# Kernel optimization log

Measured on AMD Instinct MI355X. Metric: run time of the kernel, lower is better.

Reference implementation:

```python
import jax, jax.numpy as jnp
import numpy as np
import math

B, T, C, H = 4, 2048, 1024, 16
D = C // H  # head dim = 64


def setup_inputs() -> dict:
    key = jax.random.key(0)
    ks = jax.random.split(key, 5)
    scale = 0.02
    x = jax.random.normal(ks[0], (B, T, C), dtype=jnp.float32)
    # torch nn.Linear(n_embd, 3*n_embd): weight [3C, C]; we store transposed [C, 3C]
    W_kqv = jax.random.normal(ks[1], (C, 3 * C), dtype=jnp.float32) * scale
    b_kqv = jnp.zeros((3 * C,), dtype=jnp.float32)
    W_proj = jax.random.normal(ks[2], (C, C), dtype=jnp.float32) * scale
    b_proj = jnp.zeros((C,), dtype=jnp.float32)
    padding_mask = jnp.ones((B, T), dtype=jnp.int32)  # 1 = valid token
    return {"x": x, "W_kqv": W_kqv, "b_kqv": b_kqv, "W_proj": W_proj,
            "b_proj": b_proj, "padding_mask": padding_mask}


def reference(x, W_kqv, b_kqv, W_proj, b_proj, padding_mask):
    Bx, Tx, Cx = x.shape
    kqv = x @ W_kqv + b_kqv                      # [B,T,3C]
    # original splits as k, q, v (in that order)
    k, q, v = jnp.split(kqv, 3, axis=2)
    def heads(t):
        return t.reshape(Bx, Tx, H, D).transpose(0, 2, 1, 3)  # [B,H,T,D]
    k, q, v = heads(k), heads(q), heads(v)
    att = jnp.einsum('bhqd,bhkd->bhqk', q, k) * (1.0 / math.sqrt(D))  # [B,H,T,T]
    causal = jnp.tril(jnp.ones((Tx, Tx), dtype=bool))[None, None]     # [1,1,T,T]
    valid = causal & (padding_mask[:, None, None, :] != 0)            # [B,1,T,T] broadcast
    neg_inf = jnp.finfo(att.dtype).min
    att = jnp.where(valid, att, neg_inf)
    att = jax.nn.softmax(att, axis=-1)
    y = jnp.einsum('bhqk,bhkd->bhqd', att, v)    # [B,H,T,D]
    y = y.transpose(0, 2, 1, 3).reshape(Bx, Tx, Cx)
    return y @ W_proj + b_proj
```

## Files before the change

### kernel.cpp

```cpp
#include <hip/hip_runtime.h>


typedef short bf16x8 __attribute__((ext_vector_type(8)));
typedef float floatx4 __attribute__((ext_vector_type(4)));

#define MFMA16(a, b, c) __builtin_amdgcn_mfma_f32_16x16x32_bf16(a, b, c, 0, 0, 0)

#define ASYNC_COPY16(gp, lp)                                                   \
  __builtin_amdgcn_global_load_lds(                                            \
      (__attribute__((address_space(1))) void*)(gp),                           \
      (__attribute__((address_space(3))) void*)(lp), 16, 0, 0)

#define DRAIN_VMCNT() asm volatile("s_waitcnt vmcnt(0)" ::: "memory")
#define WAIT_VMCNT6() asm volatile("s_waitcnt vmcnt(6)" ::: "memory")

#if defined(__has_builtin)
#if __has_builtin(__builtin_amdgcn_exp2f)
#define EXP2(x) __builtin_amdgcn_exp2f(x)
#endif
#endif
#ifndef EXP2
#define EXP2(x) exp2f(x)
#endif

__device__ __forceinline__ short f2bf(float f) {
  union { float f; unsigned u; } c;
  c.f = f;
  unsigned r = c.u + 0x7fffu + ((c.u >> 16) & 1u);
  return (short)(r >> 16);
}

__global__ __launch_bounds__(256) void prep(const float* __restrict__ x,
                                            short* __restrict__ xb,
                                            const float* __restrict__ Wkqv,
                                            short* __restrict__ Wkqvt,
                                            const float* __restrict__ Wproj,
                                            short* __restrict__ Wprojt) {
  __shared__ float buf[64][65];
  const int t = threadIdx.x;
  const int bx = blockIdx.x;
  if (bx < 8192) {
    int i = (bx * 256 + t) * 4;
    float4 v = *(const float4*)&x[i];
    short4 o;
    o.x = f2bf(v.x); o.y = f2bf(v.y); o.z = f2bf(v.z); o.w = f2bf(v.w);
    *(short4*)&xb[i] = o;
    return;
  }
  const int tb = bx - 8192;
  const int nb = tb & 63, kb = tb >> 6;
  const float* in;
  short* out;
  int N, n0;
  if (nb < 48) { in = Wkqv; out = Wkqvt; N = 3072; n0 = nb * 64; }
  else         { in = Wproj; out = Wprojt; N = 1024; n0 = (nb - 48) * 64; }
  const int k0 = kb * 64;
#pragma unroll
  for (int i = 0; i < 4; ++i) {
    int s = t + i * 256;
    int row = s >> 4, c4 = (s & 15) * 4;
    float4 v = *(const float4*)&in[(size_t)(k0 + row) * N + n0 + c4];
    buf[row][c4] = v.x; buf[row][c4 + 1] = v.y;
    buf[row][c4 + 2] = v.z; buf[row][c4 + 3] = v.w;
  }
  __syncthreads();
#pragma unroll
  for (int i = 0; i < 2; ++i) {
    int u = t + i * 256;
    int rn = u >> 3, ch = (u & 7) * 8;
    short tmp[8];
#pragma unroll
    for (int j = 0; j < 8; ++j) tmp[j] = f2bf(buf[ch + j][rn]);
    *(uint4*)&out[(size_t)(n0 + rn) * 1024 + k0 + ch] = *(uint4*)tmp;
  }
}

template <int MODE>
__global__ __launch_bounds__(512, 2) void gemm_ph256(const short* __restrict__ A,
                                                     const short* __restrict__ Bt,
                                                     const float* __restrict__ bias,
                                                     void* __restrict__ Cout,
                                                     int M, int N, int K) {
  __shared__ short smem[73728];
  const int tid = threadIdx.x;
  const int lane = tid & 63;
  const int wv = tid >> 6;
  const int l15 = lane & 15, quad = lane >> 4;
  const int xr = l15 & 7;
  const int m0 = blockIdx.y * 128, n0 = blockIdx.x * 256;
  const int wm = (wv >> 2) * 64, wn = (wv & 3) * 64;
  const int NT = K >> 6;

  floatx4 acc[4][4] = {};

#define STAGE_A(kt, bs, j)                                                     \
  { int c_ = (j) * 512 + tid;                                                  \
    int r_ = c_ >> 3, ch_ = (c_ & 7) ^ (r_ & 7);                               \
    ASYNC_COPY16(&A[(size_t)(m0 + r_) * K + (kt) * 64 + ch_ * 8],              \
                 &smem[(bs) * 8192 + c_ * 8]); }
#define STAGE_B(kt, bs, j)                                                     \
  { int c_ = (j) * 512 + tid;                                                  \
    int r_ = c_ >> 3, ch_ = (c_ & 7) ^ (r_ & 7);                               \
    ASYNC_COPY16(&Bt[(size_t)(n0 + r_) * K + (kt) * 64 + ch_ * 8],             \
                 &smem[24576 + (bs) * 16384 + c_ * 8]); }

  STAGE_A(0, 0, 0); STAGE_A(0, 0, 1);
  STAGE_B(0, 0, 0); STAGE_B(0, 0, 1); STAGE_B(0, 0, 2); STAGE_B(0, 0, 3);
  STAGE_A(1, 1, 0); STAGE_A(1, 1, 1);
  STAGE_B(1, 1, 0); STAGE_B(1, 1, 1); STAGE_B(1, 1, 2); STAGE_B(1, 1, 3);
  WAIT_VMCNT6();
  __builtin_amdgcn_s_barrier();

  int cur = 0, nxt = 2;
  for (int kt = 0; kt < NT; ++kt) {
    const bool st = (kt + 2 < NT);
    const short* Asr = &smem[cur * 8192];
    const short* Bsr = &smem[24576 + cur * 16384];

    if (st) { STAGE_A(kt + 2, nxt, 0); STAGE_A(kt + 2, nxt, 1); STAGE_B(kt + 2, nxt, 0); }
    bf16x8 af[4][2], bf0[2][2];
#pragma unroll
    for (int mi = 0; mi < 4; ++mi)
#pragma unroll
      for (int s = 0; s < 2; ++s)
        af[mi][s] = *(const bf16x8*)
            &Asr[(wm + mi * 16 + l15) * 64 + (((s * 4 + quad) ^ xr) * 8)];
#pragma unroll
    for (int nj = 0; nj < 2; ++nj)
#pragma unroll
      for (int s = 0; s < 2; ++s)
        bf0[nj][s] = *(const bf16x8*)
            &Bsr[(wn + nj * 16 + l15) * 64 + (((s * 4 + quad) ^ xr) * 8)];
    __builtin_amdgcn_s_setprio(1);
#pragma unroll
    for (int s = 0; s < 2; ++s)
#pragma unroll
      for (int mi = 0; mi < 4; ++mi)
#pragma unroll
        for (int nj = 0; nj < 2; ++nj)
          acc[mi][nj] = MFMA16(af[mi][s], bf0[nj][s], acc[mi][nj]);
    __builtin_amdgcn_s_setprio(0);
    __builtin_amdgcn_s_barrier();

    if (st) { STAGE_B(kt + 2, nxt, 1); STAGE_B(kt + 2, nxt, 2); STAGE_B(kt + 2, nxt, 3); }
    bf16x8 bf1[2][2];
#pragma unroll
    for (int nj = 0; nj < 2; ++nj)
#pragma unroll
      for (int s = 0; s < 2; ++s)
        bf1[nj][s] = *(const bf16x8*)
            &Bsr[(wn + (2 + nj) * 16 + l15) * 64 + (((s * 4 + quad) ^ xr) * 8)];
    __builtin_amdgcn_s_setprio(1);
#pragma unroll
    for (int s = 0; s < 2; ++s)
#pragma unroll
      for (int mi = 0; mi < 4; ++mi)
#pragma unroll
        for (int nj = 0; nj < 2; ++nj)
          acc[mi][2 + nj] = MFMA16(af[mi][s], bf1[nj][s], acc[mi][2 + nj]);
    __builtin_amdgcn_s_setprio(0);
    if (st) { WAIT_VMCNT6(); } else { DRAIN_VMCNT(); }
    __builtin_amdgcn_s_barrier();
    cur = (cur == 2) ? 0 : cur + 1;
    nxt = (nxt == 2) ? 0 : nxt + 1;
  }
#undef STAGE_A
#undef STAGE_B

  if (MODE == 0) {
    float* outf = (float*)Cout;
#pragma unroll
    for (int ni = 0; ni < 4; ++ni) {
      int col = n0 + wn + ni * 16 + l15;
      float bv = bias[col];
#pragma unroll
      for (int mi = 0; mi < 4; ++mi) {
#pragma unroll
        for (int rr = 0; rr < 4; ++rr) {
          int row = m0 + wm + mi * 16 + quad * 4 + rr;
          outf[(size_t)row * N + col] = acc[mi][ni][rr] + bv;
        }
      }
    }
  } else {
    short* outs = (short*)Cout;
    const size_t QOFF = (size_t)64 * 2048 * 64;
    const int sec = n0 >> 10;
    short* Es = smem;
    if (sec < 2) {
#pragma unroll
      for (int ni = 0; ni < 4; ++ni) {
        int c = wn + ni * 16 + l15;
        float bv = bias[n0 + c];
#pragma unroll
        for (int mi = 0; mi < 4; ++mi) {
          int r0 = wm + mi * 16 + quad * 4;
#pragma unroll
          for (int rr = 0; rr < 4; ++rr) {
            int r = r0 + rr;
            Es[r * 256 + (c ^ (((r >> 2) & 3) << 4))] = f2bf(acc[mi][ni][rr] + bv);
          }
        }
      }
    } else {
#pragma unroll
      for (int ni = 0; ni < 4; ++ni) {
        int c = wn + ni * 16 + l15;
        float bv = bias[n0 + c];
#pragma unroll
        for (int mi = 0; mi < 4; ++mi) {
          int r0 = wm + mi * 16 + quad * 4;
#pragma unroll
          for (int rr = 0; rr < 4; ++rr) {
            int r = r0 + rr;
            Es[c * 128 + (r ^ ((c & 7) << 3))] = f2bf(acc[mi][ni][rr] + bv);
          }
        }
      }
    }
    __syncthreads();
    if (sec < 2) {
#pragma unroll
      for (int jj = 0; jj < 8; ++jj) {
        int idx = jj * 512 + tid;
        int rr2 = idx >> 5;
        int cc2 = (idx & 31) * 8;
        uint4 v = *(const uint4*)&Es[rr2 * 256 + (cc2 ^ (((rr2 >> 2) & 3) << 4))];
        int colg = n0 + cc2;
        int hh = (colg >> 6) & 15, dd = colg & 63;
        int row = m0 + rr2, bb = row >> 11, tt = row & 2047;
        *(uint4*)(outs + (size_t)sec * QOFF +
                  (((size_t)(bb * 16 + hh) * 2048 + tt) * 64 + dd)) = v;
      }
    } else {
#pragma unroll
      for (int jj = 0; jj < 8; ++jj) {
        int idx = jj * 512 + tid;
        int cd = idx >> 4;
        int rb = (idx & 15) * 8;
        uint4 v = *(const uint4*)&Es[cd * 128 + (rb ^ ((cd & 7) << 3))];
        int colg = n0 + cd;
        int hh = (colg >> 6) & 15, dd = colg & 63;
        int trow = m0 + rb, bb = trow >> 11, tt = trow & 2047;
        *(uint4*)(outs + 2 * QOFF +
                  ((size_t)(bb * 16 + hh) * 64 + dd) * 2048 + tt) = v;
      }
    }
  }
}

__global__ __launch_bounds__(256, 3) void attn_flash8(const short* __restrict__ Qd,
                                                      const short* __restrict__ Kd,
                                                      const short* __restrict__ Vd,
                                                      const int* __restrict__ pmask,
                                                      short* __restrict__ y) {
  constexpr int T = 2048, C = 1024;
  __shared__ short Ks[2][64 * 64];
  __shared__ short Vs[2][64 * 64];
  __shared__ short Ps[4][32][64];

  const int tid = threadIdx.x;
  const int lane = tid & 63, w = tid >> 6;
  const int l15 = lane & 15, quad = lane >> 4;
  const int xr = l15 & 7;
  const int lin = blockIdx.x;
  const int qb = 15 - (lin >> 6);
  const int bh = lin & 63;
  const int b = bh >> 4, h = bh & 15;
  const short* Qb = Qd + (size_t)bh * T * 64;
  const short* Kb = Kd + (size_t)bh * T * 64;
  const short* Vb = Vd + (size_t)bh * 64 * T;
  const int* pmi = &pmask[b * T];
  const int q0 = qb * 128;
  const int nt = (q0 >> 6) + 2;

  const float SCALE2 = 0.18033688011112042f;

#define STAGE_KV(t, buf)                                                       \
  {                                                                            \
    const short* ksrc_ = Kb + (size_t)((t) * 64) * 64;                         \
    const short* vsrc_ = Vb + (t) * 64;                                        \
    _Pragma("unroll")                                                          \
    for (int j_ = 0; j_ < 2; ++j_) {                                           \
      int c_ = j_ * 256 + tid;                                                 \
      int r_ = c_ >> 3, cc_ = (c_ & 7) ^ (r_ & 7);                             \
      ASYNC_COPY16(ksrc_ + r_ * 64 + cc_ * 8, &Ks[buf][c_ * 8]);               \
      ASYNC_COPY16(vsrc_ + (size_t)r_ * T + cc_ * 8, &Vs[buf][c_ * 8]);        \
    }                                                                          \
  }

  bf16x8 qf[2][2];
#pragma unroll
  for (int mi = 0; mi < 2; ++mi) {
    const short* qp = Qb + (size_t)(q0 + w * 32 + mi * 16 + l15) * 64;
    qf[mi][0] = *(const bf16x8*)&qp[quad * 8];
    qf[mi][1] = *(const bf16x8*)&qp[32 + quad * 8];
  }

  floatx4 Oacc[2][4] = {};
  float lpart[2] = {};

  STAGE_KV(0, 0);
  DRAIN_VMCNT();
  __syncthreads();

  int cur = 0;
#pragma unroll 1
  for (int t = 0; t < nt; ++t) {
    const int k0 = t * 64;
    if (t + 1 < nt) STAGE_KV(t + 1, cur ^ 1);

    floatx4 Sacc[2][4] = {};
#pragma unroll
    for (int s = 0; s < 2; ++s) {
#pragma unroll
      for (int n4 = 0; n4 < 4; ++n4) {
        bf16x8 bK = *(const bf16x8*)
            &Ks[cur][(n4 * 16 + l15) * 64 + (((s * 4 + quad) ^ xr) * 8)];
        Sacc[0][n4] = MFMA16(bK, qf[0][s], Sacc[0][n4]);
        Sacc[1][n4] = MFMA16(bK, qf[1][s], Sacc[1][n4]);
      }
    }

    if (k0 < q0) {
#pragma unroll
      for (int n4 = 0; n4 < 4; ++n4) {
        int4 pm4 = *(const int4*)&pmi[k0 + n4 * 16 + quad * 4];
        float pb[4];
        pb[0] = pm4.x ? 0.0f : -3.0e38f;
        pb[1] = pm4.y ? 0.0f : -3.0e38f;
        pb[2] = pm4.z ? 0.0f : -3.0e38f;
        pb[3] = pm4.w ? 0.0f : -3.0e38f;
#pragma unroll
        for (int mi = 0; mi < 2; ++mi) {
          float p[4];
#pragma unroll
          for (int rr = 0; rr < 4; ++rr) {
            p[rr] = EXP2(fmaf(Sacc[mi][n4][rr], SCALE2, pb[rr]));
            lpart[mi] += p[rr];
          }
          unsigned lo, hi;
          asm("v_cvt_pk_bf16_f32 %0, %1, %2" : "=v"(lo) : "v"(p[0]), "v"(p[1]));
          asm("v_cvt_pk_bf16_f32 %0, %1, %2" : "=v"(hi) : "v"(p[2]), "v"(p[3]));
          uint2 pk; pk.x = lo; pk.y = hi;
          *(uint2*)&Ps[w][mi * 16 + l15]
                      [((n4 * 2 + (quad >> 1)) ^ xr) * 8 + (quad & 1) * 4] = pk;
        }
      }
    } else {
#pragma unroll
      for (int n4 = 0; n4 < 4; ++n4) {
        int4 pm4 = *(const int4*)&pmi[k0 + n4 * 16 + quad * 4];
        float pb[4];
        pb[0] = pm4.x ? 0.0f : -3.0e38f;
        pb[1] = pm4.y ? 0.0f : -3.0e38f;
        pb[2] = pm4.z ? 0.0f : -3.0e38f;
        pb[3] = pm4.w ? 0.0f : -3.0e38f;
        const int colb = n4 * 16 + quad * 4;
#pragma unroll
        for (int mi = 0; mi < 2; ++mi) {
          const int rowb = (q0 - k0) + w * 32 + mi * 16 + l15;
          float p[4];
#pragma unroll
          for (int rr = 0; rr < 4; ++rr) {
            float v = EXP2(fmaf(Sacc[mi][n4][rr], SCALE2, pb[rr]));
            if (colb + rr > rowb) v = 0.f;
            p[rr] = v;
            lpart[mi] += v;
          }
          unsigned lo, hi;
          asm("v_cvt_pk_bf16_f32 %0, %1, %2" : "=v"(lo) : "v"(p[0]), "v"(p[1]));
          asm("v_cvt_pk_bf16_f32 %0, %1, %2" : "=v"(hi) : "v"(p[2]), "v"(p[3]));
          uint2 pk; pk.x = lo; pk.y = hi;
          *(uint2*)&Ps[w][mi * 16 + l15]
                      [((n4 * 2 + (quad >> 1)) ^ xr) * 8 + (quad & 1) * 4] = pk;
        }
      }
    }

#pragma unroll
    for (int ks2 = 0; ks2 < 2; ++ks2) {
      const int pco = (((ks2 * 4 + quad) ^ xr) * 8);
      bf16x8 ap0 = *(const bf16x8*)&Ps[w][l15][pco];
      bf16x8 ap1 = *(const bf16x8*)&Ps[w][16 + l15][pco];
#pragma unroll
      for (int nd = 0; nd < 4; ++nd) {
        bf16x8 bV = *(const bf16x8*)
            &Vs[cur][(nd * 16 + l15) * 64 + (((ks2 * 4 + quad) ^ xr) * 8)];
        Oacc[0][nd] = MFMA16(ap0, bV, Oacc[0][nd]);
        Oacc[1][nd] = MFMA16(ap1, bV, Oacc[1][nd]);
      }
    }

    DRAIN_VMCNT();
    __syncthreads();
    cur ^= 1;
  }
#undef STAGE_KV

#pragma unroll
  for (int mi = 0; mi < 2; ++mi) {
    float s = lpart[mi];
    s += __shfl_xor(s, 16, 64);
    s += __shfl_xor(s, 32, 64);
    float inv_l[4];
#pragma unroll
    for (int rr = 0; rr < 4; ++rr)
      inv_l[rr] = 1.0f / __shfl(s, quad * 4 + rr, 16);
#pragma unroll
    for (int n = 0; n < 4; ++n) {
      int dcol = n * 16 + l15;
#pragma unroll
      for (int rr = 0; rr < 4; ++rr) {
        int rowq = q0 + w * 32 + mi * 16 + quad * 4 + rr;
        y[((size_t)(b * T + rowq)) * C + h * 64 + dcol] =
            f2bf(Oacc[mi][n][rr] * inv_l[rr]);
      }
    }
  }
}

extern "C" void kernel_launch(void* const* d_in, const int* in_sizes, int n_in,
                              void* d_out, int out_size, void* d_ws, size_t ws_size,
                              hipStream_t stream) {
  constexpr int B = 4, T = 2048, C = 1024;
  constexpr int M = B * T;
  constexpr int N1 = 3 * C;

  const float* x      = (const float*)d_in[0];
  const float* W_kqv  = (const float*)d_in[1];
  const float* b_kqv  = (const float*)d_in[2];
  const float* W_proj = (const float*)d_in[3];
  const float* b_proj = (const float*)d_in[4];
  const int*   pmask  = (const int*)d_in[5];
  float* out = (float*)d_out;

  const size_t QOFF = (size_t)64 * T * 64;

  short* xb     = (short*)d_ws;
  short* Wkqvt  = xb + (size_t)M * C;
  short* Wprojt = Wkqvt + (size_t)N1 * C;
  short* qkv    = Wprojt + (size_t)C * C;
  short* yb     = xb;

  short* Kd = qkv;
  short* Qd = qkv + QOFF;
  short* Vd = qkv + 2 * QOFF;

  prep<<<dim3(8192 + 1024), 256, 0, stream>>>(x, xb, W_kqv, Wkqvt, W_proj, Wprojt);

  gemm_ph256<2><<<dim3(N1 / 256, M / 128), 512, 0, stream>>>(xb, Wkqvt, b_kqv, Kd, M, N1, C);

  attn_flash8<<<dim3(1024), 256, 0, stream>>>(Qd, Kd, Vd, pmask, yb);

  gemm_ph256<0><<<dim3(C / 256, M / 128), 512, 0, stream>>>(yb, Wprojt, b_proj, out, M, C, C);
}
```

Before: 252.3 us.

## Keep softmax probabilities in registers via permlane swaps and add 128-tile output GEMM

The attention kernel no longer writes probabilities to a per-wave LDS buffer and reads them back for the PV MFMA. It reshuffles them in registers with v_permlane32_swap and shuffles, computes O transposed, and stores packed bf16 rows. A runtime probe (sem1) picks the swap semantics. The output projection now uses a new 128x128 double-buffered GEMM with 256 threads in place of the 256-wide, 512-thread triple-buffered one. This trades LDS traffic for cross-lane ops and changes the projection's tiling and occupancy.

Result: slower. 258.6 us (+2.5%).

```diff
diff --git a/kernel.cpp b/kernel.cpp
--- a/kernel.cpp
+++ b/kernel.cpp
@@ -167,22 +167,7 @@
 #undef STAGE_A
 #undef STAGE_B
 
-  if (MODE == 0) {
-    float* outf = (float*)Cout;
-#pragma unroll
-    for (int ni = 0; ni < 4; ++ni) {
-      int col = n0 + wn + ni * 16 + l15;
-      float bv = bias[col];
-#pragma unroll
-      for (int mi = 0; mi < 4; ++mi) {
-#pragma unroll
-        for (int rr = 0; rr < 4; ++rr) {
-          int row = m0 + wm + mi * 16 + quad * 4 + rr;
-          outf[(size_t)row * N + col] = acc[mi][ni][rr] + bv;
-        }
-      }
-    }
-  } else {
+  {
     short* outs = (short*)Cout;
     const size_t QOFF = (size_t)64 * 2048 * 64;
     const int sec = n0 >> 10;
@@ -249,7 +234,79 @@
   }
 }
 
-__global__ __launch_bounds__(256, 3) void attn_flash8(const short* __restrict__ Qd,
+__global__ __launch_bounds__(256, 2) void gemm_dbuf128(const short* __restrict__ A,
+                                                       const short* __restrict__ Bt,
+                                                       const float* __restrict__ bias,
+                                                       float* __restrict__ outf,
+                                                       int M, int N, int K) {
+  __shared__ short As[2][8192];
+  __shared__ short Bs[2][8192];
+  const int tid = threadIdx.x;
+  const int lane = tid & 63;
+  const int wv = tid >> 6;
+  const int l15 = lane & 15, quad = lane >> 4;
+  const int xr = l15 & 7;
+  const int m0 = blockIdx.y * 128, n0 = blockIdx.x * 128;
+  const int wm = (wv >> 1) * 64, wn = (wv & 1) * 64;
+  const int NT = K >> 6;
+
+  floatx4 acc[4][4] = {};
+
+#define STAGE_AB(kt, bs)                                                       \
+  { _Pragma("unroll")                                                          \
+    for (int j_ = 0; j_ < 4; ++j_) {                                           \
+      int c_ = j_ * 256 + tid;                                                 \
+      int r_ = c_ >> 3, ch_ = (c_ & 7) ^ (r_ & 7);                             \
+      ASYNC_COPY16(&A[(size_t)(m0 + r_) * K + (kt) * 64 + ch_ * 8],            \
+                   &As[bs][c_ * 8]);                                           \
+      ASYNC_COPY16(&Bt[(size_t)(n0 + r_) * K + (kt) * 64 + ch_ * 8],           \
+                   &Bs[bs][c_ * 8]);                                           \
+    } }
+
+  STAGE_AB(0, 0);
+  DRAIN_VMCNT();
+  __syncthreads();
+
+  int cur = 0;
+  for (int kt = 0; kt < NT; ++kt) {
+    if (kt + 1 < NT) STAGE_AB(kt + 1, cur ^ 1);
+#pragma unroll
+    for (int s = 0; s < 2; ++s) {
+      const int chs = ((s * 4 + quad) ^ xr) * 8;
+      bf16x8 af[4], bfr[4];
+#pragma unroll
+      for (int i = 0; i < 4; ++i) {
+        af[i]  = *(const bf16x8*)&As[cur][(wm + i * 16 + l15) * 64 + chs];
+        bfr[i] = *(const bf16x8*)&Bs[cur][(wn + i * 16 + l15) * 64 + chs];
+      }
+#pragma unroll
+      for (int mi = 0; mi < 4; ++mi)
+#pragma unroll
+        for (int ni = 0; ni < 4; ++ni)
+          acc[mi][ni] = MFMA16(af[mi], bfr[ni], acc[mi][ni]);
+    }
+    DRAIN_VMCNT();
+    __syncthreads();
+    cur ^= 1;
+  }
+#undef STAGE_AB
+
+#pragma unroll
+  for (int ni = 0; ni < 4; ++ni) {
+    int col = n0 + wn + ni * 16 + l15;
+    float bv = bias[col];
+#pragma unroll
+    for (int mi = 0; mi < 4; ++mi) {
+#pragma unroll
+      for (int rr = 0; rr < 4; ++rr) {
+        int row = m0 + wm + mi * 16 + quad * 4 + rr;
+        outf[(size_t)row * N + col] = acc[mi][ni][rr] + bv;
+      }
+    }
+  }
+}
+
+__global__ __launch_bounds__(256, 3) void attn_flash9(const short* __restrict__ Qd,
                                                       const short* __restrict__ Kd,
                                                       const short* __restrict__ Vd,
                                                       const int* __restrict__ pmask,
@@ -257,7 +314,6 @@
   constexpr int T = 2048, C = 1024;
   __shared__ short Ks[2][64 * 64];
   __shared__ short Vs[2][64 * 64];
-  __shared__ short Ps[4][32][64];
 
   const int tid = threadIdx.x;
   const int lane = tid & 63, w = tid >> 6;
@@ -276,6 +332,10 @@
 
   const float SCALE2 = 0.18033688011112042f;
 
+  unsigned pa = (unsigned)lane, pb = (unsigned)lane + 64u;
+  asm volatile("v_permlane32_swap_b32 %0, %1" : "+v"(pa), "+v"(pb));
+  const bool sem1 = (__shfl((int)pa, 48, 64) == 80);
+
 #define STAGE_KV(t, buf)                                                       \
   {                                                                            \
     const short* ksrc_ = Kb + (size_t)((t) * 64) * 64;                         \
@@ -297,7 +357,7 @@
     qf[mi][1] = *(const bf16x8*)&qp[32 + quad * 8];
   }
 
-  floatx4 Oacc[2][4] = {};
+  floatx4 OaccT[2][4] = {};
   float lpart[2] = {};
 
   STAGE_KV(0, 0);
@@ -322,40 +382,40 @@
       }
     }
 
+    unsigned U[2][4][2];
     if (k0 < q0) {
 #pragma unroll
       for (int n4 = 0; n4 < 4; ++n4) {
         int4 pm4 = *(const int4*)&pmi[k0 + n4 * 16 + quad * 4];
-        float pb[4];
-        pb[0] = pm4.x ? 0.0f : -3.0e38f;
-        pb[1] = pm4.y ? 0.0f : -3.0e38f;
-        pb[2] = pm4.z ? 0.0f : -3.0e38f;
-        pb[3] = pm4.w ? 0.0f : -3.0e38f;
+        float pb4[4];
+        pb4[0] = pm4.x ? 0.0f : -3.0e38f;
+        pb4[1] = pm4.y ? 0.0f : -3.0e38f;
+        pb4[2] = pm4.z ? 0.0f : -3.0e38f;
+        pb4[3] = pm4.w ? 0.0f : -3.0e38f;
 #pragma unroll
         for (int mi = 0; mi < 2; ++mi) {
           float p[4];
 #pragma unroll
           for (int rr = 0; rr < 4; ++rr) {
-            p[rr] = EXP2(fmaf(Sacc[mi][n4][rr], SCALE2, pb[rr]));
+            p[rr] = EXP2(fmaf(Sacc[mi][n4][rr], SCALE2, pb4[rr]));
             lpart[mi] += p[rr];
           }
           unsigned lo, hi;
           asm("v_cvt_pk_bf16_f32 %0, %1, %2" : "=v"(lo) : "v"(p[0]), "v"(p[1]));
           asm("v_cvt_pk_bf16_f32 %0, %1, %2" : "=v"(hi) : "v"(p[2]), "v"(p[3]));
-          uint2 pk; pk.x = lo; pk.y = hi;
-          *(uint2*)&Ps[w][mi * 16 + l15]
-                      [((n4 * 2 + (quad >> 1)) ^ xr) * 8 + (quad & 1) * 4] = pk;
+          U[mi][n4][0] = lo;
+          U[mi][n4][1] = hi;
         }
       }
     } else {
 #pragma unroll
       for (int n4 = 0; n4 < 4; ++n4) {
         int4 pm4 = *(const int4*)&pmi[k0 + n4 * 16 + quad * 4];
-        float pb[4];
-        pb[0] = pm4.x ? 0.0f : -3.0e38f;
-        pb[1] = pm4.y ? 0.0f : -3.0e38f;
-        pb[2] = pm4.z ? 0.0f : -3.0e38f;
-        pb[3] = pm4.w ? 0.0f : -3.0e38f;
+        float pb4[4];
+        pb4[0] = pm4.x ? 0.0f : -3.0e38f;
+        pb4[1] = pm4.y ? 0.0f : -3.0e38f;
+        pb4[2] = pm4.z ? 0.0f : -3.0e38f;
+        pb4[3] = pm4.w ? 0.0f : -3.0e38f;
         const int colb = n4 * 16 + quad * 4;
 #pragma unroll
         for (int mi = 0; mi < 2; ++mi) {
@@ -363,7 +423,7 @@
           float p[4];
 #pragma unroll
           for (int rr = 0; rr < 4; ++rr) {
-            float v = EXP2(fmaf(Sacc[mi][n4][rr], SCALE2, pb[rr]));
+            float v = EXP2(fmaf(Sacc[mi][n4][rr], SCALE2, pb4[rr]));
             if (colb + rr > rowb) v = 0.f;
             p[rr] = v;
             lpart[mi] += v;
@@ -371,24 +431,51 @@
           unsigned lo, hi;
           asm("v_cvt_pk_bf16_f32 %0, %1, %2" : "=v"(lo) : "v"(p[0]), "v"(p[1]));
           asm("v_cvt_pk_bf16_f32 %0, %1, %2" : "=v"(hi) : "v"(p[2]), "v"(p[3]));
-          uint2 pk; pk.x = lo; pk.y = hi;
-          *(uint2*)&Ps[w][mi * 16 + l15]
-                      [((n4 * 2 + (quad >> 1)) ^ xr) * 8 + (quad & 1) * 4] = pk;
+          U[mi][n4][0] = lo;
+          U[mi][n4][1] = hi;
         }
       }
     }
 
 #pragma unroll
     for (int ks2 = 0; ks2 < 2; ++ks2) {
-      const int pco = (((ks2 * 4 + quad) ^ xr) * 8);
-      bf16x8 ap0 = *(const bf16x8*)&Ps[w][l15][pco];
-      bf16x8 ap1 = *(const bf16x8*)&Ps[w][16 + l15][pco];
+      unsigned Wq[2][4];
+      if (sem1) {
+#pragma unroll
+        for (int mi = 0; mi < 2; ++mi)
+#pragma unroll
+          for (int hh2 = 0; hh2 < 2; ++hh2) {
+            unsigned x = U[mi][2 * ks2][hh2], yv = U[mi][2 * ks2 + 1][hh2];
+            asm volatile("v_permlane32_swap_b32 %0, %1" : "+v"(x), "+v"(yv));
+            unsigned o1 = x, o2 = yv;
+            unsigned o1x = (unsigned)__shfl_xor((int)o1, 16, 64);
+            unsigned o2x = (unsigned)__shfl_xor((int)o2, 16, 64);
+            Wq[mi][hh2]     = (quad & 1) ? o2x : o1;
+            Wq[mi][2 + hh2] = (quad & 1) ? o2 : o1x;
+          }
+      } else {
+#pragma unroll
+        for (int mi = 0; mi < 2; ++mi)
+#pragma unroll
+          for (int hh2 = 0; hh2 < 2; ++hh2) {
+            unsigned x = U[mi][2 * ks2 + 1][hh2], yv = U[mi][2 * ks2][hh2];
+            asm volatile("v_permlane32_swap_b32 %0, %1" : "+v"(x), "+v"(yv));
+            unsigned o1 = yv, o2 = x;
+            unsigned o1x = (unsigned)__shfl_xor((int)o1, 16, 64);
+            unsigned o2x = (unsigned)__shfl_xor((int)o2, 16, 64);
+            Wq[mi][hh2]     = (quad & 1) ? o2x : o1;
+            Wq[mi][2 + hh2] = (quad & 1) ? o2 : o1x;
+          }
+      }
+      union { unsigned u[4]; bf16x8 v; } w0, w1;
+#pragma unroll
+      for (int jj = 0; jj < 4; ++jj) { w0.u[jj] = Wq[0][jj]; w1.u[jj] = Wq[1][jj]; }
 #pragma unroll
       for (int nd = 0; nd < 4; ++nd) {
         bf16x8 bV = *(const bf16x8*)
             &Vs[cur][(nd * 16 + l15) * 64 + (((ks2 * 4 + quad) ^ xr) * 8)];
-        Oacc[0][nd] = MFMA16(ap0, bV, Oacc[0][nd]);
-        Oacc[1][nd] = MFMA16(ap1, bV, Oacc[1][nd]);
+        OaccT[0][nd] = MFMA16(bV, w0.v, OaccT[0][nd]);
+        OaccT[1][nd] = MFMA16(bV, w1.v, OaccT[1][nd]);
       }
     }
 
@@ -403,19 +490,18 @@
     float s = lpart[mi];
     s += __shfl_xor(s, 16, 64);
     s += __shfl_xor(s, 32, 64);
-    float inv_l[4];
-#pragma unroll
-    for (int rr = 0; rr < 4; ++rr)
-      inv_l[rr] = 1.0f / __shfl(s, quad * 4 + rr, 16);
-#pragma unroll
-    for (int n = 0; n < 4; ++n) {
-      int dcol = n * 16 + l15;
-#pragma unroll
-      for (int rr = 0; rr < 4; ++rr) {
-        int rowq = q0 + w * 32 + mi * 16 + quad * 4 + rr;
-        y[((size_t)(b * T + rowq)) * C + h * 64 + dcol] =
-            f2bf(Oacc[mi][n][rr] * inv_l[rr]);
-      }
+    float inv = 1.0f / s;
+    int rowq = q0 + w * 32 + mi * 16 + l15;
+    short* yp = &y[((size_t)(b * T + rowq)) * C + h * 64 + quad * 4];
+#pragma unroll
+    for (int nd = 0; nd < 4; ++nd) {
+      float p0 = OaccT[mi][nd][0] * inv, p1 = OaccT[mi][nd][1] * inv;
+      float p2 = OaccT[mi][nd][2] * inv, p3 = OaccT[mi][nd][3] * inv;
+      unsigned lo, hi;
+      asm("v_cvt_pk_bf16_f32 %0, %1, %2" : "=v"(lo) : "v"(p0), "v"(p1));
+      asm("v_cvt_pk_bf16_f32 %0, %1, %2" : "=v"(hi) : "v"(p2), "v"(p3));
+      uint2 pk; pk.x = lo; pk.y = hi;
+      *(uint2*)&yp[nd * 16] = pk;
     }
   }
 }
@@ -451,7 +537,7 @@
 
   gemm_ph256<2><<<dim3(N1 / 256, M / 128), 512, 0, stream>>>(xb, Wkqvt, b_kqv, Kd, M, N1, C);
 
-  attn_flash8<<<dim3(1024), 256, 0, stream>>>(Qd, Kd, Vd, pmask, yb);
-
-  gemm_ph256<0><<<dim3(C / 256, M / 128), 512, 0, stream>>>(yb, Wprojt, b_proj, out, M, C, C);
+  attn_flash9<<<dim3(1024), 256, 0, stream>>>(Qd, Kd, Vd, pmask, yb);
+
+  gemm_dbuf128<<<dim3(C / 128, M / 128), 256, 0, stream>>>(yb, Wprojt, b_proj, out, M, C, C);
 }
```
